# Kernel tuning notes

Hardware: AMD Instinct MI355X
Metric: run time of the kernel (lower is better)

## Reference

```python
import jax, jax.numpy as jnp
import numpy as np

B, N, DA, DB = 8, 2048, 768, 1024


def setup_inputs() -> dict:
    key = jax.random.key(0)
    ks = jax.random.split(key, 20)
    s = 0.02
    inp = {
        "x_a": jax.random.normal(ks[0], (B, N, DA), jnp.float32),
        "x_b": jax.random.normal(ks[1], (B, N, DB), jnp.float32),
        # self-attention params (all DB x DB), stored as [in, out]
        "sa_wq": jax.random.normal(ks[2], (DB, DB), jnp.float32) * s,
        "sa_bq": jnp.zeros((DB,), jnp.float32),
        "sa_wk": jax.random.normal(ks[3], (DB, DB), jnp.float32) * s,
        "sa_bk": jnp.zeros((DB,), jnp.float32),
        "sa_wv": jax.random.normal(ks[4], (DB, DB), jnp.float32) * s,
        "sa_bv": jnp.zeros((DB,), jnp.float32),
        "sa_wo": jax.random.normal(ks[5], (DB, DB), jnp.float32) * s,
        "sa_bo": jnp.zeros((DB,), jnp.float32),
        # cross-attention params: q maps DA->DB, rest DB->DB
        "ca_wq": jax.random.normal(ks[6], (DA, DB), jnp.float32) * s,
        "ca_bq": jnp.zeros((DB,), jnp.float32),
        "ca_wk": jax.random.normal(ks[7], (DB, DB), jnp.float32) * s,
        "ca_bk": jnp.zeros((DB,), jnp.float32),
        "ca_wv": jax.random.normal(ks[8], (DB, DB), jnp.float32) * s,
        "ca_bv": jnp.zeros((DB,), jnp.float32),
        "ca_wo": jax.random.normal(ks[9], (DB, DB), jnp.float32) * s,
        "ca_bo": jnp.zeros((DB,), jnp.float32),
    }
    return inp


def _attend(q, k, v, scale):
    # q: [B,Nq,D], k,v: [B,Nk,D]
    scores = jnp.einsum("bqd,bkd->bqk", q, k) / scale
    w = jax.nn.softmax(scores, axis=-1)
    return jnp.einsum("bqk,bkd->bqd", w, v)


def reference(x_a, x_b,
              sa_wq, sa_bq, sa_wk, sa_bk, sa_wv, sa_bv, sa_wo, sa_bo,
              ca_wq, ca_bq, ca_wk, ca_bk, ca_wv, ca_bv, ca_wo, ca_bo):
    # self-attention on x_b; scale = sqrt(embed_dim_b)
    q = x_b @ sa_wq + sa_bq
    k = x_b @ sa_wk + sa_bk
    v = x_b @ sa_wv + sa_bv
    sa_out = _attend(q, k, v, jnp.sqrt(jnp.float32(x_b.shape[-1]))) @ sa_wo + sa_bo
    x_b = x_b + sa_out
    # cross-attention: q from x_a, k/v from updated x_b; scale = sqrt(embed_dim_a)
    q = x_a @ ca_wq + ca_bq
    k = x_b @ ca_wk + ca_bk
    v = x_b @ ca_wv + ca_bv
    ca_out = _attend(q, k, v, jnp.sqrt(jnp.float32(x_a.shape[-1]))) @ ca_wo + ca_bo
    return x_b + ca_out
```

## Files before the change

kernel.cpp:

```cpp
#include <hip/hip_runtime.h>
#include <hip/hip_bf16.h>


#define AS1 __attribute__((address_space(1)))
#define AS3 __attribute__((address_space(3)))

typedef __attribute__((ext_vector_type(8))) short bf16x8;
typedef __attribute__((ext_vector_type(4))) float f32x4;

using bf = __hip_bfloat16;

__global__ __launch_bounds__(512, 1) void gemm256(
    const bf* __restrict__ A, const bf* __restrict__ BT,
    const float* __restrict__ bias, const float* __restrict__ biasB,
    const float* __restrict__ biasC,
    const float* __restrict__ resid32, const bf* __restrict__ resid16,
    bf* __restrict__ C16, bf* __restrict__ C16b, bf* __restrict__ C16c,
    float* __restrict__ C32,
    int M, int Nc, int K, float alpha,
    long sA, long sB, long sC, int tstore, int nseg)
{
    __shared__ __align__(16) char lds[131072];

    const int tid  = threadIdx.x;
    const int wave = tid >> 6;
    const int lane = tid & 63;
    const int wm = wave >> 2;
    const int wn = wave & 3;

    const int gx = gridDim.x, gy = gridDim.y;
    int wg = blockIdx.y * gx + blockIdx.x;
    const int nwg = gx * gy;
    if (!(nwg & 7)) wg = (wg & 7) * (nwg >> 3) + (wg >> 3);
    const int m0 = (wg / gx) * 256;
    const int n0 = (wg % gx) * 256;

    const long zC = (long)blockIdx.z * sC;
    A  += (long)blockIdx.z * sA;
    BT += (long)blockIdx.z * sB;

    const int fl = lane & 15, qd = lane >> 4;
    const int sr = lane >> 3;
    const int scn = (lane & 7) ^ sr;
    const long ldb = (long)K * 2;

    const char* gA = (const char*)A  + (long)(m0 + wave * 16 + sr) * ldb + scn * 16;
    const char* gB = (const char*)BT + (long)(n0 + wave * 16 + sr) * ldb + scn * 16;

    auto stage_ht = [&](int s) {
        const int t = s >> 2, r = s & 3;
        const char* g = ((r & 1) ? gB : gA) + (long)((r >> 1) * 128) * ldb + (long)t * 128;
        char* l = lds + ((t & 1) * 65536) + r * 16384 + wave * 2048;
        __builtin_amdgcn_global_load_lds((const AS1 void*)g,               (AS3 void*)l,          16, 0, 0);
        __builtin_amdgcn_global_load_lds((const AS1 void*)(g + 8 * ldb),   (AS3 void*)(l + 1024), 16, 0, 0);
    };

    const int xo = fl & 7;
    const int so0 = ((0 | qd) ^ xo) * 16;
    const int so1 = ((4 | qd) ^ xo) * 16;
    const char* Abase = lds + (wm ? 2 : 0) * 16384 + fl * 128;
    const char* Bbase = lds + ((wn >> 1) ? 3 : 1) * 16384 + (wn & 1) * 64 * 128 + fl * 128;

    f32x4 acc[8][4];
#pragma unroll
    for (int i = 0; i < 8; ++i)
#pragma unroll
        for (int j = 0; j < 4; ++j)
            acc[i][j] = (f32x4){0.f, 0.f, 0.f, 0.f};

    bf16x8 afr[2][4][2];
    bf16x8 bfr[2][2][2];

#define READ_A(mq, SL) { const char* pA_ = Abase + (SL) * 65536 + (mq) * 8192; \
    _Pragma("unroll") for (int f_ = 0; f_ < 4; ++f_) { \
        afr[mq][f_][0] = *(const bf16x8*)(pA_ + f_ * 2048 + so0); \
        afr[mq][f_][1] = *(const bf16x8*)(pA_ + f_ * 2048 + so1); } }

#define READ_B(nq, SL) { const char* pB_ = Bbase + (SL) * 65536 + (nq) * 4096; \
    _Pragma("unroll") for (int g_ = 0; g_ < 2; ++g_) { \
        bfr[nq][g_][0] = *(const bf16x8*)(pB_ + g_ * 2048 + so0); \
        bfr[nq][g_][1] = *(const bf16x8*)(pB_ + g_ * 2048 + so1); } }

#define MFMA_Q(mq, nq) { \
    __builtin_amdgcn_s_setprio(1); \
    _Pragma("unroll") for (int f_ = 0; f_ < 4; ++f_) \
    _Pragma("unroll") for (int g_ = 0; g_ < 2; ++g_) { \
        acc[(mq)*4+f_][(nq)*2+g_] = __builtin_amdgcn_mfma_f32_16x16x32_bf16( \
            afr[mq][f_][0], bfr[nq][g_][0], acc[(mq)*4+f_][(nq)*2+g_], 0, 0, 0); \
        acc[(mq)*4+f_][(nq)*2+g_] = __builtin_amdgcn_mfma_f32_16x16x32_bf16( \
            afr[mq][f_][1], bfr[nq][g_][1], acc[(mq)*4+f_][(nq)*2+g_], 0, 0, 0); } \
    __builtin_amdgcn_s_setprio(0); }

#define SB()  __builtin_amdgcn_sched_barrier(0)
#define BARS() { SB(); __builtin_amdgcn_s_barrier(); SB(); }
#define VMCNT6() asm volatile("s_waitcnt vmcnt(6)" ::: "memory")
#define VMCNT0() asm volatile("s_waitcnt vmcnt(0)" ::: "memory")
#define STG(S) { if ((S) < nht) stage_ht(S); }

    const int NT    = K >> 6;
    const int niter = NT >> 1;
    const int nht   = NT << 2;

#pragma unroll
    for (int s = 0; s < 7; ++s) stage_ht(s);
    VMCNT6();
    BARS();

    for (int I = 0; I < niter; ++I) {
        const int s0 = 8 * I + 7;
        const bool last = (I == niter - 1);
        READ_A(0, 0); READ_B(0, 0); READ_A(1, 0); READ_B(1, 0);
        STG(s0 + 0); BARS(); MFMA_Q(0, 0); BARS();
        STG(s0 + 1); BARS(); MFMA_Q(1, 1); BARS();
        STG(s0 + 2); BARS(); MFMA_Q(0, 1); BARS();
        STG(s0 + 3); BARS(); MFMA_Q(1, 0);
        if (last) { VMCNT0(); } else { VMCNT6(); }
        BARS();
        READ_A(0, 1); READ_B(0, 1); READ_A(1, 1); READ_B(1, 1);
        STG(s0 + 4); BARS(); MFMA_Q(0, 0); BARS();
        STG(s0 + 5); BARS(); MFMA_Q(1, 1); BARS();
        STG(s0 + 6); BARS(); MFMA_Q(0, 1); BARS();
        STG(s0 + 7); BARS(); MFMA_Q(1, 0);
        if (!last) { VMCNT6(); }
        BARS();
    }

    if (nseg == 1) {
        const long ldc = Nc;
#pragma unroll
        for (int i = 0; i < 8; ++i) {
#pragma unroll
            for (int j = 0; j < 4; ++j) {
#pragma unroll
                for (int r = 0; r < 4; ++r) {
                    const int row = m0 + wm * 128 + i * 16 + qd * 4 + r;
                    const int col = n0 + wn * 64 + j * 16 + fl;
                    float v = acc[i][j][r] * alpha;
                    if (bias) v += bias[col];
                    if (tstore & 1) {
                        const long idx = (long)(row >> 11) * ((long)Nc * 2048)
                                       + (long)col * 2048 + (row & 2047);
                        C16[idx] = __float2bfloat16(v);
                    } else {
                        const long idx = zC + (long)row * ldc + col;
                        if (resid32) v += resid32[idx];
                        if (resid16) v += __bfloat162float(resid16[idx]);
                        if (C16) C16[idx] = __float2bfloat16(v);
                        if (C32) C32[idx] = v;
                    }
                }
            }
        }
    } else {
        const int seg = n0 >> 10;
        bf* dst = (seg == 0) ? C16 : ((seg == 1) ? C16b : C16c);
        const float* bseg = (seg == 0) ? bias : ((seg == 1) ? biasB : biasC);
        const int trans = (tstore >> seg) & 1;
        const int cb = n0 & 1023;
#pragma unroll
        for (int i = 0; i < 8; ++i) {
#pragma unroll
            for (int j = 0; j < 4; ++j) {
#pragma unroll
                for (int r = 0; r < 4; ++r) {
                    const int row = m0 + wm * 128 + i * 16 + qd * 4 + r;
                    const int col = cb + wn * 64 + j * 16 + fl;
                    float v = acc[i][j][r] * alpha + bseg[col];
                    const long idx = trans
                        ? (long)(row >> 11) * (1024L * 2048) + (long)col * 2048 + (row & 2047)
                        : (long)row * 1024 + col;
                    dst[idx] = __float2bfloat16(v);
                }
            }
        }
    }
#undef READ_A
#undef READ_B
#undef MFMA_Q
#undef SB
#undef BARS
#undef VMCNT6
#undef VMCNT0
#undef STG
}

__global__ __launch_bounds__(256) void cast_f32_bf16(
    const float* __restrict__ in, bf* __restrict__ out, long n)
{
    long i = ((long)blockIdx.x * 256 + threadIdx.x) * 8;
    if (i >= n) return;
    float4 a = *(const float4*)(in + i);
    float4 b = *(const float4*)(in + i + 4);
    bf o[8] = {__float2bfloat16(a.x), __float2bfloat16(a.y),
               __float2bfloat16(a.z), __float2bfloat16(a.w),
               __float2bfloat16(b.x), __float2bfloat16(b.y),
               __float2bfloat16(b.z), __float2bfloat16(b.w)};
    *(bf16x8*)(out + i) = *(bf16x8*)o;
}

__global__ __launch_bounds__(256) void transpose_f32_bf16(
    const float* __restrict__ in, bf* __restrict__ out, int R, int C)
{
    __shared__ bf t[32][33];
    const int c0 = blockIdx.x * 32, r0 = blockIdx.y * 32;
    const int tx = threadIdx.x, ty = threadIdx.y;
#pragma unroll
    for (int i = ty; i < 32; i += 8)
        t[i][tx] = __float2bfloat16(in[(long)(r0 + i) * C + c0 + tx]);
    __syncthreads();
#pragma unroll
    for (int i = ty; i < 32; i += 8)
        out[(long)(c0 + i) * R + r0 + tx] = t[tx][i];
}

__global__ __launch_bounds__(256) void softmax_rows(bf* __restrict__ S)
{
    const long row = blockIdx.x;
    bf* p = S + row * 2048;
    const int tx = threadIdx.x;

    float v[8];
    float m = -3.0e38f;
#pragma unroll
    for (int i = 0; i < 8; i++) {
        v[i] = __bfloat162float(p[tx + 256 * i]);
        m = fmaxf(m, v[i]);
    }
    __shared__ float red[4];
#pragma unroll
    for (int o = 1; o < 64; o <<= 1) m = fmaxf(m, __shfl_xor(m, o, 64));
    if ((tx & 63) == 0) red[tx >> 6] = m;
    __syncthreads();
    m = fmaxf(fmaxf(red[0], red[1]), fmaxf(red[2], red[3]));

    float s = 0.f;
#pragma unroll
    for (int i = 0; i < 8; i++) { v[i] = __expf(v[i] - m); s += v[i]; }
#pragma unroll
    for (int o = 1; o < 64; o <<= 1) s += __shfl_xor(s, o, 64);
    __syncthreads();
    if ((tx & 63) == 0) red[tx >> 6] = s;
    __syncthreads();
    const float inv = 1.0f / (red[0] + red[1] + red[2] + red[3]);
#pragma unroll
    for (int i = 0; i < 8; i++) p[tx + 256 * i] = __float2bfloat16(v[i] * inv);
}

extern "C" void kernel_launch(void* const* d_in, const int* in_sizes, int n_in,
                              void* d_out, int out_size, void* d_ws, size_t ws_size,
                              hipStream_t stream)
{
    const int Bb = 8, Nn = 2048, DA = 768, DB = 1024;
    const long Mt = (long)Bb * Nn;

    const float* x_a   = (const float*)d_in[0];
    const float* x_b   = (const float*)d_in[1];
    const float* sa_wq = (const float*)d_in[2];  const float* sa_bq = (const float*)d_in[3];
    const float* sa_wk = (const float*)d_in[4];  const float* sa_bk = (const float*)d_in[5];
    const float* sa_wv = (const float*)d_in[6];  const float* sa_bv = (const float*)d_in[7];
    const float* sa_wo = (const float*)d_in[8];  const float* sa_bo = (const float*)d_in[9];
    const float* ca_wq = (const float*)d_in[10]; const float* ca_bq = (const float*)d_in[11];
    const float* ca_wk = (const float*)d_in[12]; const float* ca_bk = (const float*)d_in[13];
    const float* ca_wv = (const float*)d_in[14]; const float* ca_bv = (const float*)d_in[15];
    const float* ca_wo = (const float*)d_in[16]; const float* ca_bo = (const float*)d_in[17];
    float* out = (float*)d_out;
    (void)in_sizes; (void)n_in; (void)out_size; (void)ws_size;

    char* ws = (char*)d_ws;
    size_t off = 0;
    auto alloc = [&](size_t bytes) -> bf* {
        bf* p = (bf*)(ws + off);
        off += (bytes + 255) & ~(size_t)255;
        return p;
    };
    bf* wqkvT = alloc((size_t)3 * DB * DB * 2);
    bf* woT   = alloc((size_t)DB * DB * 2);
    bf* cwqT  = alloc((size_t)DB * DA * 2);
    bf* ckvT  = alloc((size_t)2 * DB * DB * 2);
    bf* cwoT  = alloc((size_t)DB * DB * 2);
    bf* slA   = alloc((size_t)Mt * DB * 2);
    bf* slQ   = alloc((size_t)Mt * DB * 2);
    bf* slK   = alloc((size_t)Mt * DB * 2);
    bf* slV   = alloc((size_t)Mt * DB * 2);
    bf* S     = alloc((size_t)Bb * Nn * Nn * 2);

    const dim3 tb(32, 8);
    const dim3 blk(256);
    const dim3 blk5(512);
    const long sQ = (long)Nn * DB;
    const long sS = (long)Nn * Nn;
    const float* nf = nullptr;
    const bf*    nb = nullptr;
    bf*          no = nullptr;

    transpose_f32_bf16<<<dim3(DB/32, DB/32), tb, 0, stream>>>(sa_wq, wqkvT,                 DB, DB);
    transpose_f32_bf16<<<dim3(DB/32, DB/32), tb, 0, stream>>>(sa_wk, wqkvT + (size_t)DB*DB, DB, DB);
    transpose_f32_bf16<<<dim3(DB/32, DB/32), tb, 0, stream>>>(sa_wv, wqkvT + (size_t)2*DB*DB, DB, DB);
    transpose_f32_bf16<<<dim3(DB/32, DB/32), tb, 0, stream>>>(sa_wo, woT,  DB, DB);
    transpose_f32_bf16<<<dim3(DB/32, DA/32), tb, 0, stream>>>(ca_wq, cwqT, DA, DB);
    transpose_f32_bf16<<<dim3(DB/32, DB/32), tb, 0, stream>>>(ca_wk, ckvT,                 DB, DB);
    transpose_f32_bf16<<<dim3(DB/32, DB/32), tb, 0, stream>>>(ca_wv, ckvT + (size_t)DB*DB, DB, DB);
    transpose_f32_bf16<<<dim3(DB/32, DB/32), tb, 0, stream>>>(ca_wo, cwoT, DB, DB);

    cast_f32_bf16<<<dim3((unsigned)(Mt * DB / 8 / 256)), blk, 0, stream>>>(x_b, slA, Mt * DB);
    gemm256<<<dim3(3*DB/256, Mt/256, 1), blk5, 0, stream>>>(
        slA, wqkvT, sa_bq, sa_bk, sa_bv, nf, nb, slQ, slK, slV, nullptr,
        (int)Mt, 3*DB, DB, 1.0f, 0, 0, 0, 0b100, 3);
    gemm256<<<dim3(Nn/256, Nn/256, Bb), blk5, 0, stream>>>(
        slQ, slK, nf, nf, nf, nf, nb, S, no, no, nullptr,
        Nn, Nn, DB, 0.03125f, sQ, sQ, sS, 0, 1);
    softmax_rows<<<dim3((unsigned)(Bb * Nn)), blk, 0, stream>>>(S);
    gemm256<<<dim3(DB/256, Nn/256, Bb), blk5, 0, stream>>>(
        S, slV, nf, nf, nf, nf, nb, slK, no, no, nullptr,
        Nn, DB, Nn, 1.0f, sS, sQ, sQ, 0, 1);
    gemm256<<<dim3(DB/256, Mt/256, 1), blk5, 0, stream>>>(
        slK, woT, sa_bo, nf, nf, x_b, nb, slQ, no, no, nullptr,
        (int)Mt, DB, DB, 1.0f, 0, 0, 0, 0, 1);

    cast_f32_bf16<<<dim3((unsigned)(Mt * DA / 8 / 256)), blk, 0, stream>>>(x_a, slA, Mt * DA);
    gemm256<<<dim3(DB/256, Mt/256, 1), blk5, 0, stream>>>(
        slA, cwqT, ca_bq, nf, nf, nf, nb, slK, no, no, nullptr,
        (int)Mt, DB, DA, 1.0f, 0, 0, 0, 0, 1);
    gemm256<<<dim3(2*DB/256, Mt/256, 1), blk5, 0, stream>>>(
        slQ, ckvT, ca_bk, ca_bv, nf, nf, nb, slV, slA, no, nullptr,
        (int)Mt, 2*DB, DB, 1.0f, 0, 0, 0, 0b10, 2);
    gemm256<<<dim3(Nn/256, Nn/256, Bb), blk5, 0, stream>>>(
        slK, slV, nf, nf, nf, nf, nb, S, no, no, nullptr,
        Nn, Nn, DB, 0.036084391824351615f, sQ, sQ, sS, 0, 1);
    softmax_rows<<<dim3((unsigned)(Bb * Nn)), blk, 0, stream>>>(S);
    gemm256<<<dim3(DB/256, Nn/256, Bb), blk5, 0, stream>>>(
        S, slA, nf, nf, nf, nf, nb, slV, no, no, nullptr,
        Nn, DB, Nn, 1.0f, sS, sQ, sQ, 0, 1);
    gemm256<<<dim3(DB/256, Mt/256, 1), blk5, 0, stream>>>(
        slV, cwoT, ca_bo, nf, nf, nf, slQ, no, no, no, out,
        (int)Mt, DB, DB, 1.0f, 0, 0, 0, 0, 1);
}
```

Before: 1.147 ms.

## Restructure GEMM mainloop to K=32 tiles with four-slot LDS ring pipeline

Replaces the K=64 double-buffered GEMM main loop with K=32 tiles held in a four-slot LDS ring, three tiles prefetched ahead, and a new XOR swizzle for the narrower rows. Each iteration interleaves fragment reads, one staging load per quarter, and four 8-MFMA quadrants, with graduated vmcnt waits at the tail. The goal is finer-grained overlap of global-to-LDS loads with MFMA work and smaller register fragments. In exchange it issues more barriers per unit of K and has smaller per-load transfers, which may add synchronization overhead.

```diff
diff --git a/kernel.cpp b/kernel.cpp
--- a/kernel.cpp
+++ b/kernel.cpp
@@ -40,26 +40,22 @@
     BT += (long)blockIdx.z * sB;
 
     const int fl = lane & 15, qd = lane >> 4;
-    const int sr = lane >> 3;
-    const int scn = (lane & 7) ^ sr;
     const long ldb = (long)K * 2;
 
-    const char* gA = (const char*)A  + (long)(m0 + wave * 16 + sr) * ldb + scn * 16;
-    const char* gB = (const char*)BT + (long)(n0 + wave * 16 + sr) * ldb + scn * 16;
-
-    auto stage_ht = [&](int s) {
-        const int t = s >> 2, r = s & 3;
-        const char* g = ((r & 1) ? gB : gA) + (long)((r >> 1) * 128) * ldb + (long)t * 128;
-        char* l = lds + ((t & 1) * 65536) + r * 16384 + wave * 2048;
-        __builtin_amdgcn_global_load_lds((const AS1 void*)g,               (AS3 void*)l,          16, 0, 0);
-        __builtin_amdgcn_global_load_lds((const AS1 void*)(g + 8 * ldb),   (AS3 void*)(l + 1024), 16, 0, 0);
+    const int sRow = lane >> 2;
+    const int sChk = (lane & 3) ^ ((lane >> 3) & 3);
+    const char* gA = (const char*)A  + (long)(m0 + wave * 16 + sRow) * ldb + sChk * 16;
+    const char* gB = (const char*)BT + (long)(n0 + wave * 16 + sRow) * ldb + sChk * 16;
+
+    auto stage = [&](int t, int r) {
+        const char* g = ((r & 1) ? gB : gA) + (long)((r >> 1) * 128) * ldb + (long)t * 64;
+        char* l = lds + (t & 3) * 32768 + r * 8192 + wave * 1024;
+        __builtin_amdgcn_global_load_lds((const AS1 void*)g, (AS3 void*)l, 16, 0, 0);
     };
 
-    const int xo = fl & 7;
-    const int so0 = ((0 | qd) ^ xo) * 16;
-    const int so1 = ((4 | qd) ^ xo) * 16;
-    const char* Abase = lds + (wm ? 2 : 0) * 16384 + fl * 128;
-    const char* Bbase = lds + ((wn >> 1) ? 3 : 1) * 16384 + (wn & 1) * 64 * 128 + fl * 128;
+    const int soff = ((qd ^ ((fl >> 1) & 3)) * 16);
+    const char* Abase = lds + (wm ? 2 : 0) * 8192 + fl * 64 + soff;
+    const char* Bbase = lds + ((wn >> 1) ? 3 : 1) * 8192 + (wn & 1) * 4096 + fl * 64 + soff;
 
     f32x4 acc[8][4];
 #pragma unroll
@@ -68,61 +64,60 @@
         for (int j = 0; j < 4; ++j)
             acc[i][j] = (f32x4){0.f, 0.f, 0.f, 0.f};
 
-    bf16x8 afr[2][4][2];
-    bf16x8 bfr[2][2][2];
-
-#define READ_A(mq, SL) { const char* pA_ = Abase + (SL) * 65536 + (mq) * 8192; \
-    _Pragma("unroll") for (int f_ = 0; f_ < 4; ++f_) { \
-        afr[mq][f_][0] = *(const bf16x8*)(pA_ + f_ * 2048 + so0); \
-        afr[mq][f_][1] = *(const bf16x8*)(pA_ + f_ * 2048 + so1); } }
-
-#define READ_B(nq, SL) { const char* pB_ = Bbase + (SL) * 65536 + (nq) * 4096; \
-    _Pragma("unroll") for (int g_ = 0; g_ < 2; ++g_) { \
-        bfr[nq][g_][0] = *(const bf16x8*)(pB_ + g_ * 2048 + so0); \
-        bfr[nq][g_][1] = *(const bf16x8*)(pB_ + g_ * 2048 + so1); } }
-
-#define MFMA_Q(mq, nq) { \
+    bf16x8 aLo[4], aHi[4], bLo[2], bHi[2];
+
+#define RD_ALO(SL) { const char* p_ = Abase + (SL) * 32768; \
+    _Pragma("unroll") for (int f_ = 0; f_ < 4; ++f_) aLo[f_] = *(const bf16x8*)(p_ + f_ * 1024); }
+#define RD_AHI(SL) { const char* p_ = Abase + (SL) * 32768 + 4096; \
+    _Pragma("unroll") for (int f_ = 0; f_ < 4; ++f_) aHi[f_] = *(const bf16x8*)(p_ + f_ * 1024); }
+#define RD_BLO(SL) { const char* p_ = Bbase + (SL) * 32768; \
+    _Pragma("unroll") for (int g_ = 0; g_ < 2; ++g_) bLo[g_] = *(const bf16x8*)(p_ + g_ * 1024); }
+#define RD_BHI(SL) { const char* p_ = Bbase + (SL) * 32768 + 2048; \
+    _Pragma("unroll") for (int g_ = 0; g_ < 2; ++g_) bHi[g_] = *(const bf16x8*)(p_ + g_ * 1024); }
+
+#define MFMA8(FR, RO, GR, CO) { \
     __builtin_amdgcn_s_setprio(1); \
     _Pragma("unroll") for (int f_ = 0; f_ < 4; ++f_) \
-    _Pragma("unroll") for (int g_ = 0; g_ < 2; ++g_) { \
-        acc[(mq)*4+f_][(nq)*2+g_] = __builtin_amdgcn_mfma_f32_16x16x32_bf16( \
-            afr[mq][f_][0], bfr[nq][g_][0], acc[(mq)*4+f_][(nq)*2+g_], 0, 0, 0); \
-        acc[(mq)*4+f_][(nq)*2+g_] = __builtin_amdgcn_mfma_f32_16x16x32_bf16( \
-            afr[mq][f_][1], bfr[nq][g_][1], acc[(mq)*4+f_][(nq)*2+g_], 0, 0, 0); } \
+    _Pragma("unroll") for (int g_ = 0; g_ < 2; ++g_) \
+        acc[(RO) + f_][(CO) + g_] = __builtin_amdgcn_mfma_f32_16x16x32_bf16( \
+            FR[f_], GR[g_], acc[(RO) + f_][(CO) + g_], 0, 0, 0); \
     __builtin_amdgcn_s_setprio(0); }
 
 #define SB()  __builtin_amdgcn_sched_barrier(0)
 #define BARS() { SB(); __builtin_amdgcn_s_barrier(); SB(); }
-#define VMCNT6() asm volatile("s_waitcnt vmcnt(6)" ::: "memory")
-#define VMCNT0() asm volatile("s_waitcnt vmcnt(0)" ::: "memory")
-#define STG(S) { if ((S) < nht) stage_ht(S); }
-
-    const int NT    = K >> 6;
-    const int niter = NT >> 1;
-    const int nht   = NT << 2;
-
-#pragma unroll
-    for (int s = 0; s < 7; ++s) stage_ht(s);
-    VMCNT6();
+#define VMC(N) asm volatile("s_waitcnt vmcnt(" #N ")" ::: "memory")
+
+    const int NT = K >> 5;
+
+#pragma unroll
+    for (int t = 0; t < 3; ++t)
+#pragma unroll
+        for (int r = 0; r < 4; ++r) stage(t, r);
+    VMC(8);
     BARS();
 
-    for (int I = 0; I < niter; ++I) {
-        const int s0 = 8 * I + 7;
-        const bool last = (I == niter - 1);
-        READ_A(0, 0); READ_B(0, 0); READ_A(1, 0); READ_B(1, 0);
-        STG(s0 + 0); BARS(); MFMA_Q(0, 0); BARS();
-        STG(s0 + 1); BARS(); MFMA_Q(1, 1); BARS();
-        STG(s0 + 2); BARS(); MFMA_Q(0, 1); BARS();
-        STG(s0 + 3); BARS(); MFMA_Q(1, 0);
-        if (last) { VMCNT0(); } else { VMCNT6(); }
+    for (int t = 0; t < NT; ++t) {
+        const int st = t + 3;
+        const int sl = t & 3;
+        const bool sOK = st < NT;
+        RD_ALO(sl); RD_BLO(sl);
+        if (sOK) stage(st, 0);
         BARS();
-        READ_A(0, 1); READ_B(0, 1); READ_A(1, 1); READ_B(1, 1);
-        STG(s0 + 4); BARS(); MFMA_Q(0, 0); BARS();
-        STG(s0 + 5); BARS(); MFMA_Q(1, 1); BARS();
-        STG(s0 + 6); BARS(); MFMA_Q(0, 1); BARS();
-        STG(s0 + 7); BARS(); MFMA_Q(1, 0);
-        if (!last) { VMCNT6(); }
+        MFMA8(aLo, 0, bLo, 0);
+        RD_BHI(sl);
+        if (sOK) stage(st, 1);
         BARS();
+        MFMA8(aLo, 0, bHi, 2);
+        RD_AHI(sl);
+        if (sOK) stage(st, 2);
+        BARS();
+        MFMA8(aHi, 4, bHi, 2);
+        if (sOK) stage(st, 3);
+        if (t < NT - 3)       { VMC(8); }
+        else if (t == NT - 3) { VMC(4); }
+        else                  { VMC(0); }
+        BARS();
+        MFMA8(aHi, 4, bLo, 0);
     }
 
     if (nseg == 1) {
@@ -174,14 +169,14 @@
             }
         }
     }
-#undef READ_A
-#undef READ_B
-#undef MFMA_Q
+#undef RD_ALO
+#undef RD_AHI
+#undef RD_BLO
+#undef RD_BHI
+#undef MFMA8
 #undef SB
 #undef BARS
-#undef VMCNT6
-#undef VMCNT0
-#undef STG
+#undef VMC
 }
 
 __global__ __launch_bounds__(256) void cast_f32_bf16(
```

After: 1.137 ms. About the same (-0.9%).
